# Performance work log

Measured on AMD Instinct MI355X. Metric: run time of the kernel, lower is better.

The kernel has to match this reference:

```python
import jax, jax.numpy as jnp
import numpy as np

L, B, I, H = 1024, 64, 512, 512


def setup_inputs() -> dict:
    key = jax.random.key(0)
    ks = jax.random.split(key, 12)
    s = 1.0 / np.sqrt(I + H)  # nn.Linear default init scale
    inp = {
        "x": jax.random.normal(ks[0], (L, B, I), dtype=jnp.float32),
        "h_0": jax.random.normal(ks[1], (B, H), dtype=jnp.float32),
        "C_0": jax.random.normal(ks[2], (B, H), dtype=jnp.float32),
        "W_f": jax.random.uniform(ks[3], (H, I + H), jnp.float32, -s, s),
        "b_f": jax.random.uniform(ks[4], (H,), jnp.float32, -s, s),
        "W_i": jax.random.uniform(ks[5], (H, I + H), jnp.float32, -s, s),
        "b_i": jax.random.uniform(ks[6], (H,), jnp.float32, -s, s),
        "W_c": jax.random.uniform(ks[7], (H, I + H), jnp.float32, -s, s),
        "b_c": jax.random.uniform(ks[8], (H,), jnp.float32, -s, s),
        "W_o": jax.random.uniform(ks[9], (H, I + H), jnp.float32, -s, s),
        "b_o": jax.random.uniform(ks[10], (H,), jnp.float32, -s, s),
    }
    return inp


def reference(x, h_0, C_0, W_f, b_f, W_i, b_i, W_c, b_c, W_o, b_o):
    # Fuse the 4 gate linears into one GEMM per step: [4H, I+H]
    W_all = jnp.concatenate([W_f, W_i, W_c, W_o], axis=0)   # [4H, I+H]
    b_all = jnp.concatenate([b_f, b_i, b_c, b_o], axis=0)   # [4H]

    def step(carry, x_t):
        h, C = carry
        concat = jnp.concatenate([h, x_t], axis=1)           # [B, H+I]
        gates = concat @ W_all.T + b_all                     # [B, 4H]
        f_t = jax.nn.sigmoid(gates[:, 0 * H:1 * H])
        i_t = jax.nn.sigmoid(gates[:, 1 * H:2 * H])
        g_t = jnp.tanh(gates[:, 2 * H:3 * H])
        o_t = jax.nn.sigmoid(gates[:, 3 * H:4 * H])
        C_new = f_t * C + i_t * g_t
        h_new = o_t * jnp.tanh(C_new)
        return (h_new, C_new), h_new

    _, output = jax.lax.scan(step, (h_0, C_0), x)            # [L, B, H]
    return output
```

## Files before the change

kernel.cpp:

```cpp
#include <hip/hip_runtime.h>
#include <hip/hip_bf16.h>


typedef __attribute__((ext_vector_type(8))) short bf16x8;
typedef __attribute__((ext_vector_type(4))) float f32x4;

#define NT 1024
#define NB 64
#define NH 512
#define NI 512

#define FLAGS_OFF 0
#define HX_OFF    4096
#define ZERO_BYTES 4096

#define VBITS 0x4000400040004000ULL

__device__ __forceinline__ bf16x8 pack8(float4 a, float4 b) {
    union U2 { __hip_bfloat162 h; unsigned int u; } c0, c1, c2, c3;
    c0.h = __float22bfloat162_rn(make_float2(a.x, a.y));
    c1.h = __float22bfloat162_rn(make_float2(a.z, a.w));
    c2.h = __float22bfloat162_rn(make_float2(b.x, b.y));
    c3.h = __float22bfloat162_rn(make_float2(b.z, b.w));
    union R { bf16x8 v; unsigned int u[4]; } r;
    r.u[0] = c0.u; r.u[1] = c1.u; r.u[2] = c2.u; r.u[3] = c3.u;
    return r.v;
}

__device__ __forceinline__ float sigm(float v) {
    return 1.0f / (1.0f + __expf(-v));
}
__device__ __forceinline__ float tanh_f(float v) {
    float e = __expf(-2.0f * fabsf(v));
    float r = (1.0f - e) / (1.0f + e);
    return copysignf(r, v);
}

__global__ __launch_bounds__(256, 1) void lstm_fused(
    const float* __restrict__ x,
    const float* __restrict__ h0,
    const float* __restrict__ c0,
    const float* __restrict__ Wf, const float* __restrict__ Bf,
    const float* __restrict__ Wi, const float* __restrict__ Bi,
    const float* __restrict__ Wc, const float* __restrict__ Bc,
    const float* __restrict__ Wo, const float* __restrict__ Bo,
    float* __restrict__ out,
    unsigned char* __restrict__ ws)
{
    unsigned int*   flags = (unsigned int*)(ws + FLAGS_OFF);
    unsigned short* hx    = (unsigned short*)(ws + HX_OFF);

    const int tid  = threadIdx.x;
    const int wv   = tid >> 6;
    const int lane = tid & 63;
    const int n    = lane & 15;
    const int kg   = lane >> 4;
    const int cl   = blockIdx.x & 7;
    const int wg   = blockIdx.x >> 3;

    const int jj = (wv << 2) + (n >> 2);
    const int j  = (wg << 4) + jj;
    const int g  = n & 3;

    const float* Wg = (g == 0) ? Wf : (g == 1) ? Wi : (g == 2) ? Wc : Wo;
    const float* Bg = (g == 0) ? Bf : (g == 1) ? Bi : (g == 2) ? Bc : Bo;

    const int m_a   = (n < 8) ? n : 7;
    const int bglob = cl * 8 + m_a;

    bf16x8 bfrag[32];
    {
        const float* wrow = Wg + (size_t)j * (NH + NI);
        #pragma unroll
        for (int kb = 0; kb < 32; ++kb) {
            const float* p = wrow + kb * 32 + kg * 8;
            bfrag[kb] = pack8(*(const float4*)(p), *(const float4*)(p + 4));
        }
    }
    const float bias_v = Bg[j];

    const bool active = (g == 0) && (kg < 2);
    float Cst[4];
    #pragma unroll
    for (int r = 0; r < 4; ++r)
        Cst[r] = active ? c0[(size_t)(cl * 8 + kg * 4 + r) * NH + j] : 0.0f;

    unsigned int* fb = flags + cl * 128;
    const int myflag = wg * 4 + wv;

    for (int t = 0; t < NT; ++t) {
        const float* xrow = x + ((size_t)t * NB + bglob) * NI;
        bf16x8 xfrag[16];
        #pragma unroll
        for (int q = 0; q < 16; ++q) {
            const float* p = xrow + q * 32 + kg * 8;
            xfrag[q] = pack8(*(const float4*)(p), *(const float4*)(p + 4));
        }
        f32x4 a0 = {bias_v, bias_v, bias_v, bias_v};
        f32x4 a1 = {0.f, 0.f, 0.f, 0.f};
        f32x4 a2 = {0.f, 0.f, 0.f, 0.f};
        f32x4 a3 = {0.f, 0.f, 0.f, 0.f};
        #pragma unroll
        for (int q = 0; q < 16; q += 4) {
            a0 = __builtin_amdgcn_mfma_f32_16x16x32_bf16(xfrag[q],     bfrag[16 + q],     a0, 0, 0, 0);
            a1 = __builtin_amdgcn_mfma_f32_16x16x32_bf16(xfrag[q + 1], bfrag[16 + q + 1], a1, 0, 0, 0);
            a2 = __builtin_amdgcn_mfma_f32_16x16x32_bf16(xfrag[q + 2], bfrag[16 + q + 2], a2, 0, 0, 0);
            a3 = __builtin_amdgcn_mfma_f32_16x16x32_bf16(xfrag[q + 3], bfrag[16 + q + 3], a3, 0, 0, 0);
        }

        if (t > 0) {
            const unsigned int tgt = (unsigned int)t;
            const unsigned long long* fp =
                (const unsigned long long*)fb + lane;
            int guard = 1 << 20;
            for (;;) {
                unsigned long long fv = __hip_atomic_load(
                    fp, __ATOMIC_RELAXED, __HIP_MEMORY_SCOPE_AGENT);
                bool ok = ((unsigned int)fv >= tgt) &&
                          ((unsigned int)(fv >> 32) >= tgt);
                if (__all(ok)) break;
                if (--guard == 0) break;
                __builtin_amdgcn_s_sleep(1);
            }
            __builtin_amdgcn_sched_barrier(0);
        }

        bf16x8 hfrag[16];
        if (t == 0) {
            const float* hrow = h0 + (size_t)bglob * NH;
            #pragma unroll
            for (int q = 0; q < 16; ++q) {
                const float* p = hrow + q * 32 + kg * 8;
                hfrag[q] = pack8(*(const float4*)(p), *(const float4*)(p + 4));
            }
        } else {
            const unsigned long long pm64 =
                (((t - 1) >> 1) & 1) ? ~0ULL : 0ULL;
            const unsigned short* hrow =
                hx + ((size_t)((t - 1) & 1) * NB + bglob) * NH;
            int guard = 1 << 16;
            for (;;) {
                unsigned long long acc = 0;
                #pragma unroll
                for (int q = 0; q < 16; ++q) {
                    const unsigned long long* p =
                        (const unsigned long long*)(hrow + q * 32 + kg * 8);
                    union { bf16x8 v; unsigned long long u[2]; } un;
                    unsigned long long w0 = __hip_atomic_load(
                        p, __ATOMIC_RELAXED, __HIP_MEMORY_SCOPE_AGENT) ^ pm64;
                    unsigned long long w1 = __hip_atomic_load(
                        p + 1, __ATOMIC_RELAXED, __HIP_MEMORY_SCOPE_AGENT) ^ pm64;
                    acc |= w0;
                    acc |= w1;
                    un.u[0] = w0;
                    un.u[1] = w1;
                    hfrag[q] = un.v;
                }
                if (__all((acc & VBITS) == 0ULL)) break;
                if (--guard == 0) break;
            }
            __builtin_amdgcn_sched_barrier(0);
        }

        #pragma unroll
        for (int q = 0; q < 16; q += 4) {
            a0 = __builtin_amdgcn_mfma_f32_16x16x32_bf16(hfrag[q],     bfrag[q],     a0, 0, 0, 0);
            a1 = __builtin_amdgcn_mfma_f32_16x16x32_bf16(hfrag[q + 1], bfrag[q + 1], a1, 0, 0, 0);
            a2 = __builtin_amdgcn_mfma_f32_16x16x32_bf16(hfrag[q + 2], bfrag[q + 2], a2, 0, 0, 0);
            a3 = __builtin_amdgcn_mfma_f32_16x16x32_bf16(hfrag[q + 3], bfrag[q + 3], a3, 0, 0, 0);
        }
        f32x4 acc = (a0 + a1) + (a2 + a3);

        unsigned short* hxout = hx + (size_t)(t & 1) * NB * NH;
        const unsigned int pmask = ((t >> 1) & 1) ? 0xFFFFu : 0u;
        float harr[4];
        #pragma unroll
        for (int r = 0; r < 4; ++r) {
            float fv = acc[r];
            float iv = __shfl_xor(fv, 1);
            float gv = __shfl_xor(fv, 2);
            float ov = __shfl_xor(fv, 3);
            if (active) {
                float ft = sigm(fv);
                float it = sigm(iv);
                float gt = tanh_f(gv);
                float ot = sigm(ov);
                float Cn = ft * Cst[r] + it * gt;
                Cst[r] = Cn;
                float ht = ot * tanh_f(Cn);
                harr[r] = ht;
                int m = kg * 4 + r;
                __hip_bfloat16 hb = __float2bfloat16(ht);
                unsigned short code =
                    (unsigned short)((*(unsigned short*)&hb) ^ pmask);
                __hip_atomic_store(
                    (unsigned short*)(hxout + (size_t)(cl * 8 + m) * NH + j),
                    code, __ATOMIC_RELAXED, __HIP_MEMORY_SCOPE_AGENT);
            }
        }

        __builtin_amdgcn_sched_barrier(0);
        if (lane == 0)
            __hip_atomic_store(fb + myflag, (unsigned int)(t + 1),
                               __ATOMIC_RELAXED, __HIP_MEMORY_SCOPE_AGENT);

        if (active) {
            #pragma unroll
            for (int r = 0; r < 4; ++r) {
                int m = kg * 4 + r;
                out[((size_t)t * NB + cl * 8 + m) * NH + j] = harr[r];
            }
        }
    }
}

extern "C" void kernel_launch(void* const* d_in, const int* in_sizes, int n_in,
                              void* d_out, int out_size, void* d_ws, size_t ws_size,
                              hipStream_t stream) {
    const float* x  = (const float*)d_in[0];
    const float* h0 = (const float*)d_in[1];
    const float* c0 = (const float*)d_in[2];
    const float* Wf = (const float*)d_in[3];
    const float* Bf = (const float*)d_in[4];
    const float* Wi = (const float*)d_in[5];
    const float* Bi = (const float*)d_in[6];
    const float* Wc = (const float*)d_in[7];
    const float* Bc = (const float*)d_in[8];
    const float* Wo = (const float*)d_in[9];
    const float* Bo = (const float*)d_in[10];
    float* out = (float*)d_out;

    hipMemsetAsync(d_ws, 0, ZERO_BYTES, stream);

    lstm_fused<<<dim3(256), dim3(256), 0, stream>>>(
        x, h0, c0, Wf, Bf, Wi, Bi, Wc, Bc, Wo, Bo, out,
        (unsigned char*)d_ws);
}
```

Measured before the change: 5.824 ms.

## Precompute input-gate projections in a prologue and stream them into the recurrence

Adds a prologue phase where each wave computes the x·W_x + bias gate contribution for all timesteps. It stores the results in a large workspace slice, as fp32 or bf16 depending on available workspace size. The recurrent loop then only loads the next step's precomputed value and does the h·W_h MFMAs, which takes the x loads and conversions off the per-step path. The cost is a large workspace footprint and an extra bulk pass over x. The bf16 mode also lowers the precision of the gate preactivation. If the workspace is too small it falls back to the original path, and the hx buffer is now explicitly memset before launch.

```diff
diff --git a/kernel.cpp b/kernel.cpp
--- a/kernel.cpp
+++ b/kernel.cpp
@@ -4,15 +4,19 @@
 
 typedef __attribute__((ext_vector_type(8))) short bf16x8;
 typedef __attribute__((ext_vector_type(4))) float f32x4;
+typedef __attribute__((ext_vector_type(2))) unsigned int u32x2;
 
 #define NT 1024
 #define NB 64
 #define NH 512
 #define NI 512
 
-#define FLAGS_OFF 0
-#define HX_OFF    4096
-#define ZERO_BYTES 4096
+#define FLAG_BYTES 4096
+#define HX_BYTES   (2 * NB * NH * 2)
+#define SLICE32    ((size_t)NT * 32 * 16)
+#define SLICE16    ((size_t)NT * 32 * 8)
+#define GXB32      (1024ull * SLICE32)
+#define GXB16      (1024ull * SLICE16)
 
 #define VBITS 0x4000400040004000ULL
 
@@ -35,7 +39,14 @@
     float r = (1.0f - e) / (1.0f + e);
     return copysignf(r, v);
 }
-
+__device__ __forceinline__ float bf16hi_f(unsigned int u) {
+    union { unsigned int u; float f; } c; c.u = u & 0xFFFF0000u; return c.f;
+}
+__device__ __forceinline__ float bf16lo_f(unsigned int u) {
+    union { unsigned int u; float f; } c; c.u = u << 16; return c.f;
+}
+
+template<int GXMODE>
 __global__ __launch_bounds__(256, 1) void lstm_fused(
     const float* __restrict__ x,
     const float* __restrict__ h0,
@@ -45,11 +56,10 @@
     const float* __restrict__ Wc, const float* __restrict__ Bc,
     const float* __restrict__ Wo, const float* __restrict__ Bo,
     float* __restrict__ out,
-    unsigned char* __restrict__ ws)
+    unsigned int* __restrict__ flags,
+    unsigned short* __restrict__ hx,
+    char* __restrict__ gxws)
 {
-    unsigned int*   flags = (unsigned int*)(ws + FLAGS_OFF);
-    unsigned short* hx    = (unsigned short*)(ws + HX_OFF);
-
     const int tid  = threadIdx.x;
     const int wv   = tid >> 6;
     const int lane = tid & 63;
@@ -88,24 +98,83 @@
     unsigned int* fb = flags + cl * 128;
     const int myflag = wg * 4 + wv;
 
+    char* slice = nullptr;
+    const int li = (kg << 4) + n;
+    if constexpr (GXMODE > 0) {
+        const int wid = blockIdx.x * 4 + wv;
+        slice = gxws + (size_t)wid * (GXMODE == 1 ? SLICE32 : SLICE16);
+        for (int t = 0; t < NT; ++t) {
+            const float* xrow = x + ((size_t)t * NB + bglob) * NI;
+            bf16x8 xfrag[16];
+            #pragma unroll
+            for (int q = 0; q < 16; ++q) {
+                const float* p = xrow + q * 32 + kg * 8;
+                xfrag[q] = pack8(*(const float4*)(p), *(const float4*)(p + 4));
+            }
+            f32x4 a0 = {bias_v, bias_v, bias_v, bias_v};
+            f32x4 a1 = {0.f, 0.f, 0.f, 0.f};
+            f32x4 a2 = {0.f, 0.f, 0.f, 0.f};
+            f32x4 a3 = {0.f, 0.f, 0.f, 0.f};
+            #pragma unroll
+            for (int q = 0; q < 16; q += 4) {
+                a0 = __builtin_amdgcn_mfma_f32_16x16x32_bf16(xfrag[q],     bfrag[16 + q],     a0, 0, 0, 0);
+                a1 = __builtin_amdgcn_mfma_f32_16x16x32_bf16(xfrag[q + 1], bfrag[16 + q + 1], a1, 0, 0, 0);
+                a2 = __builtin_amdgcn_mfma_f32_16x16x32_bf16(xfrag[q + 2], bfrag[16 + q + 2], a2, 0, 0, 0);
+                a3 = __builtin_amdgcn_mfma_f32_16x16x32_bf16(xfrag[q + 3], bfrag[16 + q + 3], a3, 0, 0, 0);
+            }
+            f32x4 acc = (a0 + a1) + (a2 + a3);
+            if (kg < 2) {
+                if constexpr (GXMODE == 1) {
+                    *(f32x4*)(slice + ((size_t)t * 32 + li) * 16) = acc;
+                } else {
+                    union { __hip_bfloat162 h; unsigned int u; } p0, p1;
+                    p0.h = __float22bfloat162_rn(make_float2(acc[0], acc[1]));
+                    p1.h = __float22bfloat162_rn(make_float2(acc[2], acc[3]));
+                    u32x2 v = {p0.u, p1.u};
+                    *(u32x2*)(slice + ((size_t)t * 32 + li) * 8) = v;
+                }
+            }
+        }
+        asm volatile("s_waitcnt vmcnt(0)" ::: "memory");
+    }
+
+    f32x4 gxv = {0.f, 0.f, 0.f, 0.f};
+    if constexpr (GXMODE == 1) {
+        if (kg < 2) gxv = *(const f32x4*)(slice + (size_t)li * 16);
+    } else if constexpr (GXMODE == 2) {
+        if (kg < 2) {
+            u32x2 v = *(const u32x2*)(slice + (size_t)li * 8);
+            gxv[0] = bf16lo_f(v.x); gxv[1] = bf16hi_f(v.x);
+            gxv[2] = bf16lo_f(v.y); gxv[3] = bf16hi_f(v.y);
+        }
+    }
+
     for (int t = 0; t < NT; ++t) {
-        const float* xrow = x + ((size_t)t * NB + bglob) * NI;
-        bf16x8 xfrag[16];
-        #pragma unroll
-        for (int q = 0; q < 16; ++q) {
-            const float* p = xrow + q * 32 + kg * 8;
-            xfrag[q] = pack8(*(const float4*)(p), *(const float4*)(p + 4));
-        }
-        f32x4 a0 = {bias_v, bias_v, bias_v, bias_v};
-        f32x4 a1 = {0.f, 0.f, 0.f, 0.f};
-        f32x4 a2 = {0.f, 0.f, 0.f, 0.f};
-        f32x4 a3 = {0.f, 0.f, 0.f, 0.f};
-        #pragma unroll
-        for (int q = 0; q < 16; q += 4) {
-            a0 = __builtin_amdgcn_mfma_f32_16x16x32_bf16(xfrag[q],     bfrag[16 + q],     a0, 0, 0, 0);
-            a1 = __builtin_amdgcn_mfma_f32_16x16x32_bf16(xfrag[q + 1], bfrag[16 + q + 1], a1, 0, 0, 0);
-            a2 = __builtin_amdgcn_mfma_f32_16x16x32_bf16(xfrag[q + 2], bfrag[16 + q + 2], a2, 0, 0, 0);
-            a3 = __builtin_amdgcn_mfma_f32_16x16x32_bf16(xfrag[q + 3], bfrag[16 + q + 3], a3, 0, 0, 0);
+        f32x4 a0, a1, a2, a3;
+        if constexpr (GXMODE == 0) {
+            const float* xrow = x + ((size_t)t * NB + bglob) * NI;
+            bf16x8 xfrag[16];
+            #pragma unroll
+            for (int q = 0; q < 16; ++q) {
+                const float* p = xrow + q * 32 + kg * 8;
+                xfrag[q] = pack8(*(const float4*)(p), *(const float4*)(p + 4));
+            }
+            a0 = (f32x4){bias_v, bias_v, bias_v, bias_v};
+            a1 = (f32x4){0.f, 0.f, 0.f, 0.f};
+            a2 = (f32x4){0.f, 0.f, 0.f, 0.f};
+            a3 = (f32x4){0.f, 0.f, 0.f, 0.f};
+            #pragma unroll
+            for (int q = 0; q < 16; q += 4) {
+                a0 = __builtin_amdgcn_mfma_f32_16x16x32_bf16(xfrag[q],     bfrag[16 + q],     a0, 0, 0, 0);
+                a1 = __builtin_amdgcn_mfma_f32_16x16x32_bf16(xfrag[q + 1], bfrag[16 + q + 1], a1, 0, 0, 0);
+                a2 = __builtin_amdgcn_mfma_f32_16x16x32_bf16(xfrag[q + 2], bfrag[16 + q + 2], a2, 0, 0, 0);
+                a3 = __builtin_amdgcn_mfma_f32_16x16x32_bf16(xfrag[q + 3], bfrag[16 + q + 3], a3, 0, 0, 0);
+            }
+        } else {
+            a0 = gxv;
+            a1 = (f32x4){0.f, 0.f, 0.f, 0.f};
+            a2 = (f32x4){0.f, 0.f, 0.f, 0.f};
+            a3 = (f32x4){0.f, 0.f, 0.f, 0.f};
         }
 
         if (t > 0) {
@@ -140,7 +209,7 @@
                 hx + ((size_t)((t - 1) & 1) * NB + bglob) * NH;
             int guard = 1 << 16;
             for (;;) {
-                unsigned long long acc = 0;
+                unsigned long long accb = 0;
                 #pragma unroll
                 for (int q = 0; q < 16; ++q) {
                     const unsigned long long* p =
@@ -150,13 +219,13 @@
                         p, __ATOMIC_RELAXED, __HIP_MEMORY_SCOPE_AGENT) ^ pm64;
                     unsigned long long w1 = __hip_atomic_load(
                         p + 1, __ATOMIC_RELAXED, __HIP_MEMORY_SCOPE_AGENT) ^ pm64;
-                    acc |= w0;
-                    acc |= w1;
+                    accb |= w0;
+                    accb |= w1;
                     un.u[0] = w0;
                     un.u[1] = w1;
                     hfrag[q] = un.v;
                 }
-                if (__all((acc & VBITS) == 0ULL)) break;
+                if (__all((accb & VBITS) == 0ULL)) break;
                 if (--guard == 0) break;
             }
             __builtin_amdgcn_sched_barrier(0);
@@ -211,6 +280,19 @@
                 out[((size_t)t * NB + cl * 8 + m) * NH + j] = harr[r];
             }
         }
+
+        if constexpr (GXMODE == 1) {
+            int tn = (t + 1 < NT) ? t + 1 : NT - 1;
+            if (kg < 2)
+                gxv = *(const f32x4*)(slice + ((size_t)tn * 32 + li) * 16);
+        } else if constexpr (GXMODE == 2) {
+            int tn = (t + 1 < NT) ? t + 1 : NT - 1;
+            if (kg < 2) {
+                u32x2 v = *(const u32x2*)(slice + ((size_t)tn * 32 + li) * 8);
+                gxv[0] = bf16lo_f(v.x); gxv[1] = bf16hi_f(v.x);
+                gxv[2] = bf16lo_f(v.y); gxv[3] = bf16hi_f(v.y);
+            }
+        }
     }
 }
 
@@ -230,9 +312,27 @@
     const float* Bo = (const float*)d_in[10];
     float* out = (float*)d_out;
 
-    hipMemsetAsync(d_ws, 0, ZERO_BYTES, stream);
-
-    lstm_fused<<<dim3(256), dim3(256), 0, stream>>>(
-        x, h0, c0, Wf, Bf, Wi, Bi, Wc, Bc, Wo, Bo, out,
-        (unsigned char*)d_ws);
-}
+    int mode;
+    size_t gxb;
+    if      (ws_size >= GXB32 + FLAG_BYTES + HX_BYTES) { mode = 1; gxb = GXB32; }
+    else if (ws_size >= GXB16 + FLAG_BYTES + HX_BYTES) { mode = 2; gxb = GXB16; }
+    else                                               { mode = 0; gxb = 0;     }
+
+    char*           ws    = (char*)d_ws;
+    char*           gxws  = ws;
+    unsigned int*   flags = (unsigned int*)(ws + gxb);
+    unsigned short* hx    = (unsigned short*)(ws + gxb + FLAG_BYTES);
+
+    hipMemsetAsync(flags, 0, FLAG_BYTES, stream);
+    hipMemsetAsync(hx, 0x7F, HX_BYTES, stream);
+
+    if (mode == 1)
+        lstm_fused<1><<<dim3(256), dim3(256), 0, stream>>>(
+            x, h0, c0, Wf, Bf, Wi, Bi, Wc, Bc, Wo, Bo, out, flags, hx, gxws);
+    else if (mode == 2)
+        lstm_fused<2><<<dim3(256), dim3(256), 0, stream>>>(
+            x, h0, c0, Wf, Bf, Wi, Bi, Wc, Bc, Wo, Bo, out, flags, hx, gxws);
+    else
+        lstm_fused<0><<<dim3(256), dim3(256), 0, stream>>>(
+            x, h0, c0, Wf, Bf, Wi, Bi, Wc, Bc, Wo, Bo, out, flags, hx, gxws);
+}
```

Measured after the change: 15.41 ms. +164.5%, slower.
